# Optimization experiments

Measured on AMD Instinct MI355X. Metric: run time of the kernel, lower is better.

## Reference

```python
import jax, jax.numpy as jnp
import numpy as np

MODEL_DIM = 512
NUM_HEADS = 16
D_OUTPUT = 128
DIM_PER_HEAD = MODEL_DIM // NUM_HEADS  # 32
LN_EPS = 1e-5


def setup_inputs() -> dict:
    key = jax.random.key(0)
    ks = jax.random.split(key, 12)
    B = 128
    proj = MODEL_DIM * D_OUTPUT  # 65536
    s = 0.02
    return {
        "key": jax.random.normal(ks[0], (B, 1, MODEL_DIM), jnp.float32),
        "value": jax.random.normal(ks[1], (B, 1, MODEL_DIM), jnp.float32),
        "query": jax.random.normal(ks[2], (B, 1, MODEL_DIM), jnp.float32),
        "Wk": jax.random.normal(ks[3], (MODEL_DIM, proj), jnp.float32) * s,
        "bk": jnp.zeros((proj,), jnp.float32),
        "Wv": jax.random.normal(ks[4], (MODEL_DIM, proj), jnp.float32) * s,
        "bv": jnp.zeros((proj,), jnp.float32),
        "Wq": jax.random.normal(ks[5], (MODEL_DIM, proj), jnp.float32) * s,
        "bq": jnp.zeros((proj,), jnp.float32),
        "Wo": jax.random.normal(ks[6], (MODEL_DIM, MODEL_DIM), jnp.float32) * s,
        "bo": jnp.zeros((MODEL_DIM,), jnp.float32),
        "gamma": jnp.ones((MODEL_DIM,), jnp.float32),
        "beta": jnp.zeros((MODEL_DIM,), jnp.float32),
    }


def reference(key, value, query, Wk, bk, Wv, bv, Wq, bq, Wo, bo, gamma, beta):
    B = key.shape[0]
    residual = query  # [B, 1, model_dim]
    # QKV projections to model_dim*d_output, then view as (B*H, d_output, dim_per_head)
    k = (key @ Wk + bk).reshape(B * NUM_HEADS, -1, DIM_PER_HEAD)
    v = (value @ Wv + bv).reshape(B * NUM_HEADS, -1, DIM_PER_HEAD)
    q = (query @ Wq + bq).reshape(B * NUM_HEADS, -1, DIM_PER_HEAD)
    # faithful to original: scale = (dim_per_head // num_heads) ** -0.5 (int div)
    scale = (DIM_PER_HEAD // NUM_HEADS) ** (-0.5)
    scores = jnp.einsum('bqd,bkd->bqk', q, k) * scale  # [B*H, S, S]
    attn = jax.nn.softmax(scores, axis=2)
    context = jnp.einsum('bqk,bkd->bqd', attn, v)  # [B*H, S, dph]
    context = context.reshape(B, -1, DIM_PER_HEAD * NUM_HEADS)  # [B, d_output, model_dim]
    out = context @ Wo + bo
    x = residual + out  # broadcast [B,1,D] + [B,d_output,D]
    mu = jnp.mean(x, axis=-1, keepdims=True)
    var = jnp.mean(jnp.square(x - mu), axis=-1, keepdims=True)
    out = (x - mu) * jax.lax.rsqrt(var + LN_EPS) * gamma + beta
    return out, attn
```

## Files before the change

### kernel.cpp

```cpp
#include <hip/hip_runtime.h>

typedef unsigned short u16;
typedef unsigned int u32;
typedef __attribute__((ext_vector_type(4))) float f32x4;
typedef __attribute__((ext_vector_type(4))) u16 u16x4;
typedef __attribute__((ext_vector_type(8))) u16 u16x8;
typedef __attribute__((ext_vector_type(8))) __bf16 bf16x8;

#define DEV static __device__ __forceinline__

DEV u16 f2b(float f) {
  u32 u = __builtin_bit_cast(u32, f);
  u32 r = (u + 0x7fffu + ((u >> 16) & 1u)) >> 16;
  return (u16)r;
}

DEV bf16x8 mk8(u16x4 lo, u16x4 hi) {
  u16x8 v = __builtin_shufflevector(lo, hi, 0, 1, 2, 3, 4, 5, 6, 7);
  return __builtin_bit_cast(bf16x8, v);
}

__global__ __launch_bounds__(256) void qkv_proj(
    const float* __restrict__ key, const float* __restrict__ value, const float* __restrict__ query,
    const float* __restrict__ Wk, const float* __restrict__ bk,
    const float* __restrict__ Wv, const float* __restrict__ bv,
    const float* __restrict__ Wq, const float* __restrict__ bq,
    u16* __restrict__ Kp, u16* __restrict__ Vp, u16* __restrict__ Qp)
{
  const int mat = blockIdx.y;
  const float* X    = mat == 0 ? key : (mat == 1 ? value : query);
  const float* W    = mat == 0 ? Wk  : (mat == 1 ? Wv    : Wq);
  const float* bias = mat == 0 ? bk  : (mat == 1 ? bv    : bq);
  u16* out          = mat == 0 ? Kp  : (mat == 1 ? Vp    : Qp);
  const int n0 = blockIdx.x * 128;

  __shared__ u16 As[16 * 512];
  __shared__ u16 Bs[16 * 512];

  const int t = threadIdx.x;
  const int lane = t & 63, wid = t >> 6;
  const int wm = wid >> 1, wn = wid & 1;
  const int l15 = lane & 15, lg = lane >> 4;

  f32x4 acc[4][4];
#pragma unroll
  for (int i = 0; i < 4; ++i)
#pragma unroll
    for (int j = 0; j < 4; ++j) acc[i][j] = (f32x4){0.f, 0.f, 0.f, 0.f};

  for (int it = 0; it < 8; ++it) {
    const int k0 = it * 64;
#pragma unroll
    for (int p = 0; p < 8; ++p) {
      int idx = p * 256 + t;
      int m = idx >> 4, kq = idx & 15;
      f32x4 xv = *(const f32x4*)(X + m * 512 + k0 + kq * 4);
      u16x4 uv;
      uv[0] = f2b(xv[0]); uv[1] = f2b(xv[1]); uv[2] = f2b(xv[2]); uv[3] = f2b(xv[3]);
      *(u16x4*)(As + kq * 512 + (((m + 2 * kq) & 127) << 2)) = uv;
    }
#pragma unroll
    for (int p = 0; p < 8; ++p) {
      int idx = p * 256 + t;
      int n = idx & 127, kq = idx >> 7;
      const float* wp = W + (size_t)(k0 + kq * 4) * 65536 + n0 + n;
      u16x4 uv;
      uv[0] = f2b(wp[0]);
      uv[1] = f2b(wp[65536]);
      uv[2] = f2b(wp[2 * 65536]);
      uv[3] = f2b(wp[3 * 65536]);
      *(u16x4*)(Bs + kq * 512 + n * 4) = uv;
    }
    __syncthreads();
#pragma unroll
    for (int kstep = 0; kstep < 2; ++kstep) {
      const int kqA = kstep * 8 + lg * 2;
      bf16x8 af[4], bfr[4];
#pragma unroll
      for (int mf = 0; mf < 4; ++mf) {
        int m = wm * 64 + mf * 16 + l15;
        u16x4 lo = *(const u16x4*)(As + kqA * 512 + (((m + 2 * kqA) & 127) << 2));
        u16x4 hi = *(const u16x4*)(As + (kqA + 1) * 512 + (((m + 2 * (kqA + 1)) & 127) << 2));
        af[mf] = mk8(lo, hi);
      }
#pragma unroll
      for (int nf = 0; nf < 4; ++nf) {
        int n = wn * 64 + nf * 16 + l15;
        u16x4 lo = *(const u16x4*)(Bs + kqA * 512 + n * 4);
        u16x4 hi = *(const u16x4*)(Bs + (kqA + 1) * 512 + n * 4);
        bfr[nf] = mk8(lo, hi);
      }
#pragma unroll
      for (int mf = 0; mf < 4; ++mf)
#pragma unroll
        for (int nf = 0; nf < 4; ++nf)
          acc[mf][nf] = __builtin_amdgcn_mfma_f32_16x16x32_bf16(af[mf], bfr[nf], acc[mf][nf], 0, 0, 0);
    }
    __syncthreads();
  }

#pragma unroll
  for (int nf = 0; nf < 4; ++nf) {
    int col = wn * 64 + nf * 16 + l15;
    float bv_ = bias[n0 + col];
#pragma unroll
    for (int mf = 0; mf < 4; ++mf) {
      int row0 = wm * 64 + mf * 16 + lg * 4;
#pragma unroll
      for (int r = 0; r < 4; ++r) {
        out[(size_t)(row0 + r) * 65536 + n0 + col] = f2b(acc[mf][nf][r] + bv_);
      }
    }
  }
}

__global__ __launch_bounds__(256) void attn_kernel(
    const u16* __restrict__ Qp, const u16* __restrict__ Kp, const u16* __restrict__ Vp,
    float* __restrict__ attnOut, u16* __restrict__ ctx)
{
  const int bh = blockIdx.x;
  const int b = bh >> 4, h = bh & 15;
  const size_t base = (size_t)b * 65536 + h * 4096;

  __shared__ u16 qS[8 * 512];
  __shared__ u16 kS[8 * 512];
  __shared__ u16 vS[32 * 128];
  __shared__ u16 pS[32 * 512];

  const int t = threadIdx.x;
  const int lane = t & 63, w = t >> 6;
  const int l15 = lane & 15, lg = lane >> 4;

#pragma unroll
  for (int p = 0; p < 2; ++p) {
    int idx = p * 256 + t;
    int s = idx >> 2, dc = idx & 3;
    u16x8 qv = *(const u16x8*)(Qp + base + s * 32 + dc * 8);
    u16x8 kv = *(const u16x8*)(Kp + base + s * 32 + dc * 8);
    u16x8 vv = *(const u16x8*)(Vp + base + s * 32 + dc * 8);
    *(u16x4*)(qS + (dc * 2) * 512 + s * 4)     = __builtin_shufflevector(qv, qv, 0, 1, 2, 3);
    *(u16x4*)(qS + (dc * 2 + 1) * 512 + s * 4) = __builtin_shufflevector(qv, qv, 4, 5, 6, 7);
    *(u16x4*)(kS + (dc * 2) * 512 + s * 4)     = __builtin_shufflevector(kv, kv, 0, 1, 2, 3);
    *(u16x4*)(kS + (dc * 2 + 1) * 512 + s * 4) = __builtin_shufflevector(kv, kv, 4, 5, 6, 7);
#pragma unroll
    for (int i = 0; i < 8; ++i)
      vS[(s >> 2) * 128 + (dc * 8 + i) * 4 + (s & 3)] = vv[i];
  }
  __syncthreads();

  f32x4 sc[2][8];
#pragma unroll
  for (int i = 0; i < 2; ++i)
#pragma unroll
    for (int j = 0; j < 8; ++j) sc[i][j] = (f32x4){0.f, 0.f, 0.f, 0.f};

  {
    const int kqA = lg * 2;
    bf16x8 aq[2];
#pragma unroll
    for (int mf = 0; mf < 2; ++mf) {
      int m = w * 32 + mf * 16 + l15;
      u16x4 lo = *(const u16x4*)(qS + kqA * 512 + m * 4);
      u16x4 hi = *(const u16x4*)(qS + (kqA + 1) * 512 + m * 4);
      aq[mf] = mk8(lo, hi);
    }
#pragma unroll
    for (int nf = 0; nf < 8; ++nf) {
      int j = nf * 16 + l15;
      u16x4 lo = *(const u16x4*)(kS + kqA * 512 + j * 4);
      u16x4 hi = *(const u16x4*)(kS + (kqA + 1) * 512 + j * 4);
      bf16x8 bk8 = mk8(lo, hi);
#pragma unroll
      for (int mf = 0; mf < 2; ++mf)
        sc[mf][nf] = __builtin_amdgcn_mfma_f32_16x16x32_bf16(aq[mf], bk8, sc[mf][nf], 0, 0, 0);
    }
  }

  const float SCL = 0.70710678118654752f;
#pragma unroll
  for (int mf = 0; mf < 2; ++mf) {
#pragma unroll
    for (int r = 0; r < 4; ++r) {
      float m8 = -1e30f;
#pragma unroll
      for (int nf = 0; nf < 8; ++nf) m8 = fmaxf(m8, sc[mf][nf][r]);
      m8 = fmaxf(m8, __shfl_xor(m8, 1));
      m8 = fmaxf(m8, __shfl_xor(m8, 2));
      m8 = fmaxf(m8, __shfl_xor(m8, 4));
      m8 = fmaxf(m8, __shfl_xor(m8, 8));
      float s8 = 0.f;
#pragma unroll
      for (int nf = 0; nf < 8; ++nf) {
        float pv = __expf((sc[mf][nf][r] - m8) * SCL);
        sc[mf][nf][r] = pv;
        s8 += pv;
      }
      s8 += __shfl_xor(s8, 1);
      s8 += __shfl_xor(s8, 2);
      s8 += __shfl_xor(s8, 4);
      s8 += __shfl_xor(s8, 8);
      float inv = 1.0f / s8;
      int i = w * 32 + mf * 16 + lg * 4 + r;
      float* ao = attnOut + (size_t)bh * 16384 + (size_t)i * 128;
#pragma unroll
      for (int nf = 0; nf < 8; ++nf) {
        int j = nf * 16 + l15;
        float pv = sc[mf][nf][r] * inv;
        ao[j] = pv;
        pS[(j >> 2) * 512 + i * 4 + (j & 3)] = f2b(pv);
      }
    }
  }
  __syncthreads();

  f32x4 cacc[2][2];
#pragma unroll
  for (int i = 0; i < 2; ++i)
#pragma unroll
    for (int j = 0; j < 2; ++j) cacc[i][j] = (f32x4){0.f, 0.f, 0.f, 0.f};

#pragma unroll
  for (int ks2 = 0; ks2 < 4; ++ks2) {
    const int kqP = ks2 * 8 + lg * 2;
    bf16x8 ap[2];
#pragma unroll
    for (int mf = 0; mf < 2; ++mf) {
      int i = w * 32 + mf * 16 + l15;
      u16x4 lo = *(const u16x4*)(pS + kqP * 512 + i * 4);
      u16x4 hi = *(const u16x4*)(pS + (kqP + 1) * 512 + i * 4);
      ap[mf] = mk8(lo, hi);
    }
#pragma unroll
    for (int nf = 0; nf < 2; ++nf) {
      int d = nf * 16 + l15;
      u16x4 lo = *(const u16x4*)(vS + kqP * 128 + d * 4);
      u16x4 hi = *(const u16x4*)(vS + (kqP + 1) * 128 + d * 4);
      bf16x8 bv8 = mk8(lo, hi);
#pragma unroll
      for (int mf = 0; mf < 2; ++mf)
        cacc[mf][nf] = __builtin_amdgcn_mfma_f32_16x16x32_bf16(ap[mf], bv8, cacc[mf][nf], 0, 0, 0);
    }
  }

#pragma unroll
  for (int mf = 0; mf < 2; ++mf) {
#pragma unroll
    for (int r = 0; r < 4; ++r) {
      int s = w * 32 + mf * 16 + lg * 4 + r;
      size_t rowbase = ((size_t)b * 128 + h * 8 + (s >> 4)) * 512 + (s & 15) * 32;
#pragma unroll
      for (int nf = 0; nf < 2; ++nf) {
        int d = nf * 16 + l15;
        ctx[rowbase + d] = f2b(cacc[mf][nf][r]);
      }
    }
  }
}

__global__ __launch_bounds__(256) void out_proj(
    const u16* __restrict__ ctx, const float* __restrict__ Wo, const float* __restrict__ bo,
    const float* __restrict__ query, float* __restrict__ pre)
{
  const int m0 = blockIdx.x * 128;
  const int n0 = blockIdx.y * 128;

  __shared__ u16 As[16 * 512];
  __shared__ u16 Bs[16 * 512];

  const int t = threadIdx.x;
  const int lane = t & 63, wid = t >> 6;
  const int wm = wid >> 1, wn = wid & 1;
  const int l15 = lane & 15, lg = lane >> 4;

  f32x4 acc[4][4];
#pragma unroll
  for (int i = 0; i < 4; ++i)
#pragma unroll
    for (int j = 0; j < 4; ++j) acc[i][j] = (f32x4){0.f, 0.f, 0.f, 0.f};

  for (int it = 0; it < 8; ++it) {
    const int k0 = it * 64;
#pragma unroll
    for (int p = 0; p < 4; ++p) {
      int idx = p * 256 + t;
      int m = idx >> 3, dc = idx & 7;
      u16x8 av = *(const u16x8*)(ctx + (size_t)(m0 + m) * 512 + k0 + dc * 8);
      int kq = dc * 2;
      *(u16x4*)(As + kq * 512 + (((m + 2 * kq) & 127) << 2)) =
          __builtin_shufflevector(av, av, 0, 1, 2, 3);
      *(u16x4*)(As + (kq + 1) * 512 + (((m + 2 * (kq + 1)) & 127) << 2)) =
          __builtin_shufflevector(av, av, 4, 5, 6, 7);
    }
#pragma unroll
    for (int p = 0; p < 8; ++p) {
      int idx = p * 256 + t;
      int n = idx & 127, kq = idx >> 7;
      const float* wp = Wo + (size_t)(k0 + kq * 4) * 512 + n0 + n;
      u16x4 uv;
      uv[0] = f2b(wp[0]);
      uv[1] = f2b(wp[512]);
      uv[2] = f2b(wp[1024]);
      uv[3] = f2b(wp[1536]);
      *(u16x4*)(Bs + kq * 512 + n * 4) = uv;
    }
    __syncthreads();
#pragma unroll
    for (int kstep = 0; kstep < 2; ++kstep) {
      const int kqA = kstep * 8 + lg * 2;
      bf16x8 af[4], bfr[4];
#pragma unroll
      for (int mf = 0; mf < 4; ++mf) {
        int m = wm * 64 + mf * 16 + l15;
        u16x4 lo = *(const u16x4*)(As + kqA * 512 + (((m + 2 * kqA) & 127) << 2));
        u16x4 hi = *(const u16x4*)(As + (kqA + 1) * 512 + (((m + 2 * (kqA + 1)) & 127) << 2));
        af[mf] = mk8(lo, hi);
      }
#pragma unroll
      for (int nf = 0; nf < 4; ++nf) {
        int n = wn * 64 + nf * 16 + l15;
        u16x4 lo = *(const u16x4*)(Bs + kqA * 512 + n * 4);
        u16x4 hi = *(const u16x4*)(Bs + (kqA + 1) * 512 + n * 4);
        bfr[nf] = mk8(lo, hi);
      }
#pragma unroll
      for (int mf = 0; mf < 4; ++mf)
#pragma unroll
        for (int nf = 0; nf < 4; ++nf)
          acc[mf][nf] = __builtin_amdgcn_mfma_f32_16x16x32_bf16(af[mf], bfr[nf], acc[mf][nf], 0, 0, 0);
    }
    __syncthreads();
  }

#pragma unroll
  for (int nf = 0; nf < 4; ++nf) {
    int col = wn * 64 + nf * 16 + l15;
    float bv_ = bo[n0 + col];
#pragma unroll
    for (int mf = 0; mf < 4; ++mf) {
      int row0 = wm * 64 + mf * 16 + lg * 4;
#pragma unroll
      for (int r = 0; r < 4; ++r) {
        int m = m0 + row0 + r;
        float res = query[(m >> 7) * 512 + n0 + col];
        pre[(size_t)m * 512 + n0 + col] = acc[mf][nf][r] + bv_ + res;
      }
    }
  }
}

__global__ __launch_bounds__(256) void ln_kernel(
    const float* __restrict__ pre, const float* __restrict__ gamma,
    const float* __restrict__ beta, float* __restrict__ out0)
{
  const int w = threadIdx.x >> 6, lane = threadIdx.x & 63;
  const int row = blockIdx.x * 4 + w;
  const float* x = pre + (size_t)row * 512;
  f32x4 v0 = *(const f32x4*)(x + lane * 8);
  f32x4 v1 = *(const f32x4*)(x + lane * 8 + 4);
  float s = v0[0] + v0[1] + v0[2] + v0[3] + v1[0] + v1[1] + v1[2] + v1[3];
  float q = v0[0] * v0[0] + v0[1] * v0[1] + v0[2] * v0[2] + v0[3] * v0[3] +
            v1[0] * v1[0] + v1[1] * v1[1] + v1[2] * v1[2] + v1[3] * v1[3];
#pragma unroll
  for (int m = 1; m < 64; m <<= 1) {
    s += __shfl_xor(s, m);
    q += __shfl_xor(q, m);
  }
  float mean = s * (1.f / 512.f);
  float var = q * (1.f / 512.f) - mean * mean;
  float rs = rsqrtf(var + 1e-5f);
  f32x4 g0 = *(const f32x4*)(gamma + lane * 8);
  f32x4 g1 = *(const f32x4*)(gamma + lane * 8 + 4);
  f32x4 b0 = *(const f32x4*)(beta + lane * 8);
  f32x4 b1 = *(const f32x4*)(beta + lane * 8 + 4);
  f32x4 o0, o1;
#pragma unroll
  for (int i = 0; i < 4; ++i) {
    o0[i] = (v0[i] - mean) * rs * g0[i] + b0[i];
    o1[i] = (v1[i] - mean) * rs * g1[i] + b1[i];
  }
  *(f32x4*)(out0 + (size_t)row * 512 + lane * 8) = o0;
  *(f32x4*)(out0 + (size_t)row * 512 + lane * 8 + 4) = o1;
}

extern "C" void kernel_launch(void* const* d_in, const int* in_sizes, int n_in,
                              void* d_out, int out_size, void* d_ws, size_t ws_size,
                              hipStream_t stream) {
  (void)in_sizes; (void)n_in; (void)out_size; (void)ws_size;
  const float* key   = (const float*)d_in[0];
  const float* value = (const float*)d_in[1];
  const float* query = (const float*)d_in[2];
  const float* Wk    = (const float*)d_in[3];
  const float* bk    = (const float*)d_in[4];
  const float* Wv    = (const float*)d_in[5];
  const float* bv    = (const float*)d_in[6];
  const float* Wq    = (const float*)d_in[7];
  const float* bq    = (const float*)d_in[8];
  const float* Wo    = (const float*)d_in[9];
  const float* bo    = (const float*)d_in[10];
  const float* gamma = (const float*)d_in[11];
  const float* beta  = (const float*)d_in[12];

  char* ws = (char*)d_ws;
  u16* Kp  = (u16*)(ws + 0);
  u16* Vp  = (u16*)(ws + 16777216);
  u16* Qp  = (u16*)(ws + 33554432);
  u16* ctx = (u16*)(ws + 50331648);
  float* pre = (float*)(ws + 0);

  float* out0    = (float*)d_out;
  float* attnOut = out0 + 8388608;

  qkv_proj<<<dim3(512, 3), 256, 0, stream>>>(key, value, query, Wk, bk, Wv, bv, Wq, bq, Kp, Vp, Qp);
  attn_kernel<<<dim3(2048), 256, 0, stream>>>(Qp, Kp, Vp, attnOut, ctx);
  out_proj<<<dim3(128, 4), 256, 0, stream>>>(ctx, Wo, bo, query, pre);
  ln_kernel<<<dim3(4096), 256, 0, stream>>>(pre, gamma, beta, out0);
}
```

Before: 193.7 us.

## Pre-convert inputs to bf16 and load QKV GEMM operands directly into registers

```diff
diff --git a/kernel.cpp b/kernel.cpp
--- a/kernel.cpp
+++ b/kernel.cpp
@@ -20,27 +20,39 @@
   return __builtin_bit_cast(bf16x8, v);
 }
 
-__global__ __launch_bounds__(256) void qkv_proj(
-    const float* __restrict__ key, const float* __restrict__ value, const float* __restrict__ query,
+__global__ __launch_bounds__(256) void prep_x(
+    const float* __restrict__ key, const float* __restrict__ value,
+    const float* __restrict__ query, u16* __restrict__ Xb)
+{
+  int idx = blockIdx.x * 256 + threadIdx.x;
+  int mat = idx >> 14;
+  int off = (idx & 16383) * 4;
+  const float* src = mat == 0 ? key : (mat == 1 ? value : query);
+  f32x4 v = *(const f32x4*)(src + off);
+  u16x4 o;
+#pragma unroll
+  for (int i = 0; i < 4; ++i) o[i] = __builtin_bit_cast(u16, (__bf16)v[i]);
+  *(u16x4*)(Xb + mat * 65536 + off) = o;
+}
+
+__global__ __launch_bounds__(256, 2) void qkv_gemm(
+    const u16* __restrict__ Xb,
     const float* __restrict__ Wk, const float* __restrict__ bk,
     const float* __restrict__ Wv, const float* __restrict__ bv,
     const float* __restrict__ Wq, const float* __restrict__ bq,
     u16* __restrict__ Kp, u16* __restrict__ Vp, u16* __restrict__ Qp)
 {
   const int mat = blockIdx.y;
-  const float* X    = mat == 0 ? key : (mat == 1 ? value : query);
-  const float* W    = mat == 0 ? Wk  : (mat == 1 ? Wv    : Wq);
-  const float* bias = mat == 0 ? bk  : (mat == 1 ? bv    : bq);
-  u16* out          = mat == 0 ? Kp  : (mat == 1 ? Vp    : Qp);
+  const float* W    = mat == 0 ? Wk : (mat == 1 ? Wv : Wq);
+  const float* bias = mat == 0 ? bk : (mat == 1 ? bv : bq);
+  u16* out          = mat == 0 ? Kp : (mat == 1 ? Vp : Qp);
+  const u16* Xm = Xb + mat * 65536;
   const int n0 = blockIdx.x * 128;
 
-  __shared__ u16 As[16 * 512];
-  __shared__ u16 Bs[16 * 512];
-
-  const int t = threadIdx.x;
-  const int lane = t & 63, wid = t >> 6;
+  const int t = threadIdx.x, lane = t & 63, wid = t >> 6;
   const int wm = wid >> 1, wn = wid & 1;
   const int l15 = lane & 15, lg = lane >> 4;
+  const int col0 = n0 + wn * 64 + l15;
 
   f32x4 acc[4][4];
 #pragma unroll
@@ -48,55 +60,33 @@
 #pragma unroll
     for (int j = 0; j < 4; ++j) acc[i][j] = (f32x4){0.f, 0.f, 0.f, 0.f};
 
-  for (int it = 0; it < 8; ++it) {
-    const int k0 = it * 64;
-#pragma unroll
-    for (int p = 0; p < 8; ++p) {
-      int idx = p * 256 + t;
-      int m = idx >> 4, kq = idx & 15;
-      f32x4 xv = *(const f32x4*)(X + m * 512 + k0 + kq * 4);
-      u16x4 uv;
-      uv[0] = f2b(xv[0]); uv[1] = f2b(xv[1]); uv[2] = f2b(xv[2]); uv[3] = f2b(xv[3]);
-      *(u16x4*)(As + kq * 512 + (((m + 2 * kq) & 127) << 2)) = uv;
-    }
-#pragma unroll
-    for (int p = 0; p < 8; ++p) {
-      int idx = p * 256 + t;
-      int n = idx & 127, kq = idx >> 7;
-      const float* wp = W + (size_t)(k0 + kq * 4) * 65536 + n0 + n;
-      u16x4 uv;
-      uv[0] = f2b(wp[0]);
-      uv[1] = f2b(wp[65536]);
-      uv[2] = f2b(wp[2 * 65536]);
-      uv[3] = f2b(wp[3 * 65536]);
-      *(u16x4*)(Bs + kq * 512 + n * 4) = uv;
-    }
-    __syncthreads();
-#pragma unroll
-    for (int kstep = 0; kstep < 2; ++kstep) {
-      const int kqA = kstep * 8 + lg * 2;
-      bf16x8 af[4], bfr[4];
-#pragma unroll
-      for (int mf = 0; mf < 4; ++mf) {
-        int m = wm * 64 + mf * 16 + l15;
-        u16x4 lo = *(const u16x4*)(As + kqA * 512 + (((m + 2 * kqA) & 127) << 2));
-        u16x4 hi = *(const u16x4*)(As + (kqA + 1) * 512 + (((m + 2 * (kqA + 1)) & 127) << 2));
-        af[mf] = mk8(lo, hi);
-      }
-#pragma unroll
-      for (int nf = 0; nf < 4; ++nf) {
-        int n = wn * 64 + nf * 16 + l15;
-        u16x4 lo = *(const u16x4*)(Bs + kqA * 512 + n * 4);
-        u16x4 hi = *(const u16x4*)(Bs + (kqA + 1) * 512 + n * 4);
-        bfr[nf] = mk8(lo, hi);
-      }
-#pragma unroll
-      for (int mf = 0; mf < 4; ++mf)
-#pragma unroll
-        for (int nf = 0; nf < 4; ++nf)
-          acc[mf][nf] = __builtin_amdgcn_mfma_f32_16x16x32_bf16(af[mf], bfr[nf], acc[mf][nf], 0, 0, 0);
-    }
-    __syncthreads();
+#pragma unroll 2
+  for (int ks = 0; ks < 16; ++ks) {
+    const int krow = ks * 32 + lg * 8;
+    bf16x8 af[4];
+#pragma unroll
+    for (int mf = 0; mf < 4; ++mf)
+      af[mf] = *(const bf16x8*)(Xm + (wm * 64 + mf * 16 + l15) * 512 + krow);
+    float bb[8][4];
+#pragma unroll
+    for (int j = 0; j < 8; ++j) {
+      const float* Wr = W + (size_t)(krow + j) * 65536 + col0;
+#pragma unroll
+      for (int nf = 0; nf < 4; ++nf) bb[j][nf] = Wr[nf * 16];
+    }
+    bf16x8 bfr[4];
+#pragma unroll
+    for (int nf = 0; nf < 4; ++nf) {
+      bf16x8 v;
+#pragma unroll
+      for (int j = 0; j < 8; ++j) v[j] = (__bf16)bb[j][nf];
+      bfr[nf] = v;
+    }
+#pragma unroll
+    for (int mf = 0; mf < 4; ++mf)
+#pragma unroll
+      for (int nf = 0; nf < 4; ++nf)
+        acc[mf][nf] = __builtin_amdgcn_mfma_f32_16x16x32_bf16(af[mf], bfr[nf], acc[mf][nf], 0, 0, 0);
   }
 
 #pragma unroll
@@ -405,12 +395,14 @@
   u16* Vp  = (u16*)(ws + 16777216);
   u16* Qp  = (u16*)(ws + 33554432);
   u16* ctx = (u16*)(ws + 50331648);
+  u16* Xb  = (u16*)(ws + 50331648);
   float* pre = (float*)(ws + 0);
 
   float* out0    = (float*)d_out;
   float* attnOut = out0 + 8388608;
 
-  qkv_proj<<<dim3(512, 3), 256, 0, stream>>>(key, value, query, Wk, bk, Wv, bv, Wq, bq, Kp, Vp, Qp);
+  prep_x<<<dim3(192), 256, 0, stream>>>(key, value, query, Xb);
+  qkv_gemm<<<dim3(512, 3), 256, 0, stream>>>(Xb, Wk, bk, Wv, bv, Wq, bq, Kp, Vp, Qp);
   attn_kernel<<<dim3(2048), 256, 0, stream>>>(Qp, Kp, Vp, attnOut, ctx);
   out_proj<<<dim3(128, 4), 256, 0, stream>>>(ctx, Wo, bo, query, pre);
   ln_kernel<<<dim3(4096), 256, 0, stream>>>(pre, gamma, beta, out0);
```

Result: slower. 230.8 us (+19.2%).
